# Kernel tuning notes

Hardware: AMD Instinct MI355X
Metric: run time of the kernel (lower is better)

The kernel has to match this reference:

```python
import jax, jax.numpy as jnp
import numpy as np

N_DROPOUT = 1      # init kwarg n_dropout
MIN_TOKENS = 10    # init kwarg min_tokens
# dynamic_dropout = False


def setup_inputs() -> dict:
    key = jax.random.key(0)
    k1, k2 = jax.random.split(key)
    B, S, V = 8192, 2048, 32000
    tokens = jax.random.randint(k1, (B, S), 1, V, dtype=jnp.int32)
    lengths = jax.random.randint(k2, (B,), 5, S + 1, dtype=jnp.int32)
    # contiguous prefix of positive token ids, 0-padded tail (as the module assumes)
    valid = jnp.arange(S, dtype=jnp.int32)[None, :] < lengths[:, None]
    input_ids = jnp.where(valid, tokens, 0)
    return {"input_ids": input_ids}


def reference(input_ids):
    # Vectorized equivalent of the per-row Python loop (training mode):
    # for every odd row with n_tokens >= MIN_TOKENS, zero N_DROPOUT random
    # token positions among the first n_tokens, then compact nonzeros left.
    B, S = input_ids.shape
    key = jax.random.key(42)

    n_tokens = jnp.sum(input_ids > 0, axis=1)  # [B]

    # random selection of N_DROPOUT distinct valid positions per row
    # (equivalent in distribution to randperm(n_tokens)[:N_DROPOUT])
    r = jax.random.uniform(key, (B, S))
    pos = jnp.arange(S)
    r = jnp.where(pos[None, :] < n_tokens[:, None], r, jnp.inf)
    _, drop_idx = jax.lax.top_k(-r, N_DROPOUT)  # [B, N_DROPOUT] smallest r
    drop_mask = jnp.zeros((B, S), dtype=bool).at[
        jnp.arange(B)[:, None], drop_idx
    ].set(True)

    apply_row = (jnp.arange(B) % 2 == 1) & (n_tokens >= MIN_TOKENS)  # [B]

    dropped = jnp.where(drop_mask & apply_row[:, None], 0, input_ids)

    # compaction: stable sort keys (zero-ness) -> nonzeros keep order, zeros go last
    order = jnp.argsort(dropped == 0, axis=1, stable=True)
    compacted = jnp.take_along_axis(dropped, order, axis=1)

    return jnp.where(apply_row[:, None], compacted, input_ids)
```

## Files before the change

### kernel.cpp

```cpp
#include <hip/hip_runtime.h>

#define PRNG_VARIANT 1

constexpr int S = 2048;
constexpr int BLOCK = 256;
constexpr int PER_THREAD = S / BLOCK;

__device__ __forceinline__ unsigned rotl32(unsigned x, int r) {
    return (x << r) | (x >> (32 - r));
}

__device__ __forceinline__ void threefry2x32_k42(unsigned c0, unsigned c1,
                                                 unsigned& o0, unsigned& o1) {
    const unsigned ks0 = 0u;
    const unsigned ks1 = 42u;
    const unsigned ks2 = 0x1BD11BDAu ^ ks0 ^ ks1;
    unsigned x0 = c0 + ks0;
    unsigned x1 = c1 + ks1;
#define TF_R4(a, b, c, d)                                   \
    x0 += x1; x1 = rotl32(x1, a); x1 ^= x0;                 \
    x0 += x1; x1 = rotl32(x1, b); x1 ^= x0;                 \
    x0 += x1; x1 = rotl32(x1, c); x1 ^= x0;                 \
    x0 += x1; x1 = rotl32(x1, d); x1 ^= x0;
    TF_R4(13, 15, 26, 6)   x0 += ks1; x1 += ks2 + 1u;
    TF_R4(17, 29, 16, 24)  x0 += ks2; x1 += ks0 + 2u;
    TF_R4(13, 15, 26, 6)   x0 += ks0; x1 += ks1 + 3u;
    TF_R4(17, 29, 16, 24)  x0 += ks1; x1 += ks2 + 4u;
    TF_R4(13, 15, 26, 6)   x0 += ks2; x1 += ks0 + 5u;
#undef TF_R4
    o0 = x0;
    o1 = x1;
}

__device__ __forceinline__ unsigned prng_bits(unsigned flat_idx, unsigned half) {
    unsigned o0, o1;
#if PRNG_VARIANT == 0
    threefry2x32_k42(0u, flat_idx, o0, o1);
    return o0;
#elif PRNG_VARIANT == 1
    threefry2x32_k42(0u, flat_idx, o0, o1);
    return o0 ^ o1;
#elif PRNG_VARIANT == 3
    threefry2x32_k42(0u, flat_idx, o0, o1);
    return o1;
#else
    if (flat_idx < half) {
        threefry2x32_k42(flat_idx, flat_idx + half, o0, o1);
        return o0;
    } else {
        threefry2x32_k42(flat_idx - half, flat_idx, o0, o1);
        return o1;
    }
#endif
}

__global__ __launch_bounds__(BLOCK) void random_dropout_kernel(
    const int* __restrict__ in, int* __restrict__ out, unsigned half_total) {
    __shared__ int row[S];
    __shared__ int wcnt[BLOCK / 64];
    __shared__ unsigned long long wmin[BLOCK / 64];
    __shared__ int s_ntok;
    __shared__ int s_drop;

    const int b = blockIdx.x;
    const size_t base = (size_t)b * S;
    const int4* vin = (const int4*)(in + base);
    int4* vout = (int4*)(out + base);
    const int tid = threadIdx.x;

    int4 v[2];
    int cnt = 0;
#pragma unroll
    for (int k = 0; k < 2; k++) {
        v[k] = vin[tid + k * BLOCK];
        ((int4*)row)[tid + k * BLOCK] = v[k];
        cnt += (v[k].x > 0) + (v[k].y > 0) + (v[k].z > 0) + (v[k].w > 0);
    }
#pragma unroll
    for (int off = 32; off; off >>= 1) cnt += __shfl_down(cnt, off, 64);
    if ((tid & 63) == 0) wcnt[tid >> 6] = cnt;
    __syncthreads();
    if (tid == 0) s_ntok = wcnt[0] + wcnt[1] + wcnt[2] + wcnt[3];
    __syncthreads();
    const int ntok = s_ntok;
    const bool apply = (b & 1) && (ntok >= 10);

    if (!apply) {
#pragma unroll
        for (int k = 0; k < 2; k++) vout[tid + k * BLOCK] = v[k];
        return;
    }

    unsigned long long best = ~0ull;
    for (int k = 0; k < PER_THREAD; k++) {
        const int s = tid + k * BLOCK;
        if (s >= ntok) break;
        const unsigned i = (unsigned)(b * S + s);
        const unsigned bits = prng_bits(i, half_total);
        const unsigned long long comb =
            ((unsigned long long)(bits >> 9) << 11) | (unsigned)s;
        best = comb < best ? comb : best;
    }
#pragma unroll
    for (int off = 32; off; off >>= 1) {
        const unsigned long long o = __shfl_down(best, off, 64);
        best = o < best ? o : best;
    }
    if ((tid & 63) == 0) wmin[tid >> 6] = best;
    __syncthreads();
    if (tid == 0) {
        unsigned long long m = wmin[0];
        m = wmin[1] < m ? wmin[1] : m;
        m = wmin[2] < m ? wmin[2] : m;
        m = wmin[3] < m ? wmin[3] : m;
        s_drop = (int)(m & 0x7FFull);
    }
    __syncthreads();
    const int drop = s_drop;

#pragma unroll
    for (int k = 0; k < 2; k++) {
        const int j4 = tid + k * BLOCK;
        const int jb = j4 * 4;
        int4 o;
        int* op = (int*)&o;
#pragma unroll
        for (int c = 0; c < 4; c++) {
            const int j = jb + c;
            int val;
            if (j < drop) val = row[j];
            else if (j < ntok - 1) val = row[j + 1];
            else val = 0;
            op[c] = val;
        }
        vout[j4] = o;
    }
}

extern "C" void kernel_launch(void* const* d_in, const int* in_sizes, int n_in,
                              void* d_out, int out_size, void* d_ws, size_t ws_size,
                              hipStream_t stream) {
    const int* in = (const int*)d_in[0];
    int* out = (int*)d_out;
    const int total = in_sizes[0];
    const int B = total / S;
    const unsigned half_total = (unsigned)(total / 2);
    random_dropout_kernel<<<B, BLOCK, 0, stream>>>(in, out, half_total);
}
```

Measured before the change: 122.2 us.

## Process one row per wavefront and replace shared-memory shifting with lane shuffles

Each 64-lane wave now owns a whole row, with four rows per block, so counting, the argmin reduction and broadcast use only wave shuffles and drop the shared memory and block barriers. The compaction shift is done in registers with cross-lane shuffles instead of a shared-memory row copy. The unused PRNG variants are removed. Each lane now holds 8 int4 values and runs up to 32 threefry evaluations serially, which raises register pressure and per-lane latency. The launch also assumes B is divisible by four.

Result: faster. 118.0 us (-3.4%).

```diff
diff --git a/kernel.cpp b/kernel.cpp
--- a/kernel.cpp
+++ b/kernel.cpp
@@ -1,22 +1,21 @@
 #include <hip/hip_runtime.h>
 
-#define PRNG_VARIANT 1
 
 constexpr int S = 2048;
 constexpr int BLOCK = 256;
-constexpr int PER_THREAD = S / BLOCK;
+constexpr int ROWS_PER_BLOCK = 4;
+constexpr int CHUNKS = S / 4 / 64;
 
 __device__ __forceinline__ unsigned rotl32(unsigned x, int r) {
     return (x << r) | (x >> (32 - r));
 }
 
-__device__ __forceinline__ void threefry2x32_k42(unsigned c0, unsigned c1,
-                                                 unsigned& o0, unsigned& o1) {
+__device__ __forceinline__ unsigned prng_bits(unsigned flat_idx) {
     const unsigned ks0 = 0u;
     const unsigned ks1 = 42u;
     const unsigned ks2 = 0x1BD11BDAu ^ ks0 ^ ks1;
-    unsigned x0 = c0 + ks0;
-    unsigned x1 = c1 + ks1;
+    unsigned x0 = 0u + ks0;
+    unsigned x1 = flat_idx + ks1;
 #define TF_R4(a, b, c, d)                                   \
     x0 += x1; x1 = rotl32(x1, a); x1 ^= x0;                 \
     x0 += x1; x1 = rotl32(x1, b); x1 ^= x0;                 \
@@ -28,75 +27,40 @@
     TF_R4(17, 29, 16, 24)  x0 += ks1; x1 += ks2 + 4u;
     TF_R4(13, 15, 26, 6)   x0 += ks2; x1 += ks0 + 5u;
 #undef TF_R4
-    o0 = x0;
-    o1 = x1;
-}
-
-__device__ __forceinline__ unsigned prng_bits(unsigned flat_idx, unsigned half) {
-    unsigned o0, o1;
-#if PRNG_VARIANT == 0
-    threefry2x32_k42(0u, flat_idx, o0, o1);
-    return o0;
-#elif PRNG_VARIANT == 1
-    threefry2x32_k42(0u, flat_idx, o0, o1);
-    return o0 ^ o1;
-#elif PRNG_VARIANT == 3
-    threefry2x32_k42(0u, flat_idx, o0, o1);
-    return o1;
-#else
-    if (flat_idx < half) {
-        threefry2x32_k42(flat_idx, flat_idx + half, o0, o1);
-        return o0;
-    } else {
-        threefry2x32_k42(flat_idx - half, flat_idx, o0, o1);
-        return o1;
-    }
-#endif
+    return x0 ^ x1;
 }
 
 __global__ __launch_bounds__(BLOCK) void random_dropout_kernel(
-    const int* __restrict__ in, int* __restrict__ out, unsigned half_total) {
-    __shared__ int row[S];
-    __shared__ int wcnt[BLOCK / 64];
-    __shared__ unsigned long long wmin[BLOCK / 64];
-    __shared__ int s_ntok;
-    __shared__ int s_drop;
-
-    const int b = blockIdx.x;
+    const int* __restrict__ in, int* __restrict__ out) {
+    const int wave = threadIdx.x >> 6;
+    const int lane = threadIdx.x & 63;
+    const int b = blockIdx.x * ROWS_PER_BLOCK + wave;
     const size_t base = (size_t)b * S;
     const int4* vin = (const int4*)(in + base);
     int4* vout = (int4*)(out + base);
-    const int tid = threadIdx.x;
 
-    int4 v[2];
+    int4 v[CHUNKS];
     int cnt = 0;
 #pragma unroll
-    for (int k = 0; k < 2; k++) {
-        v[k] = vin[tid + k * BLOCK];
-        ((int4*)row)[tid + k * BLOCK] = v[k];
+    for (int k = 0; k < CHUNKS; k++) {
+        v[k] = vin[lane + 64 * k];
         cnt += (v[k].x > 0) + (v[k].y > 0) + (v[k].z > 0) + (v[k].w > 0);
     }
 #pragma unroll
     for (int off = 32; off; off >>= 1) cnt += __shfl_down(cnt, off, 64);
-    if ((tid & 63) == 0) wcnt[tid >> 6] = cnt;
-    __syncthreads();
-    if (tid == 0) s_ntok = wcnt[0] + wcnt[1] + wcnt[2] + wcnt[3];
-    __syncthreads();
-    const int ntok = s_ntok;
+    const int ntok = __shfl(cnt, 0, 64);
+
     const bool apply = (b & 1) && (ntok >= 10);
-
     if (!apply) {
 #pragma unroll
-        for (int k = 0; k < 2; k++) vout[tid + k * BLOCK] = v[k];
+        for (int k = 0; k < CHUNKS; k++) vout[lane + 64 * k] = v[k];
         return;
     }
 
     unsigned long long best = ~0ull;
-    for (int k = 0; k < PER_THREAD; k++) {
-        const int s = tid + k * BLOCK;
-        if (s >= ntok) break;
-        const unsigned i = (unsigned)(b * S + s);
-        const unsigned bits = prng_bits(i, half_total);
+    const unsigned rowbase = (unsigned)b * (unsigned)S;
+    for (int s = lane; s < ntok; s += 64) {
+        const unsigned bits = prng_bits(rowbase + (unsigned)s);
         const unsigned long long comb =
             ((unsigned long long)(bits >> 9) << 11) | (unsigned)s;
         best = comb < best ? comb : best;
@@ -106,34 +70,26 @@
         const unsigned long long o = __shfl_down(best, off, 64);
         best = o < best ? o : best;
     }
-    if ((tid & 63) == 0) wmin[tid >> 6] = best;
-    __syncthreads();
-    if (tid == 0) {
-        unsigned long long m = wmin[0];
-        m = wmin[1] < m ? wmin[1] : m;
-        m = wmin[2] < m ? wmin[2] : m;
-        m = wmin[3] < m ? wmin[3] : m;
-        s_drop = (int)(m & 0x7FFull);
+    const unsigned long long m = __shfl(best, 0, 64);
+    const int drop = (int)(m & 0x7FFull);
+
+    int nx[CHUNKS];
+#pragma unroll
+    for (int k = 0; k < CHUNKS; k++) {
+        const int a = __shfl_down(v[k].x, 1, 64);
+        const int bb = (k < CHUNKS - 1) ? __shfl(v[k + 1].x, 0, 64) : 0;
+        nx[k] = (lane == 63) ? bb : a;
     }
-    __syncthreads();
-    const int drop = s_drop;
 
 #pragma unroll
-    for (int k = 0; k < 2; k++) {
-        const int j4 = tid + k * BLOCK;
-        const int jb = j4 * 4;
+    for (int k = 0; k < CHUNKS; k++) {
+        const int j0 = 4 * (lane + 64 * k);
         int4 o;
-        int* op = (int*)&o;
-#pragma unroll
-        for (int c = 0; c < 4; c++) {
-            const int j = jb + c;
-            int val;
-            if (j < drop) val = row[j];
-            else if (j < ntok - 1) val = row[j + 1];
-            else val = 0;
-            op[c] = val;
-        }
-        vout[j4] = o;
+        o.x = (j0 + 0 < drop) ? v[k].x : v[k].y;
+        o.y = (j0 + 1 < drop) ? v[k].y : v[k].z;
+        o.z = (j0 + 2 < drop) ? v[k].z : v[k].w;
+        o.w = (j0 + 3 < drop) ? v[k].w : nx[k];
+        vout[lane + 64 * k] = o;
     }
 }
 
@@ -144,6 +100,5 @@
     int* out = (int*)d_out;
     const int total = in_sizes[0];
     const int B = total / S;
-    const unsigned half_total = (unsigned)(total / 2);
-    random_dropout_kernel<<<B, BLOCK, 0, stream>>>(in, out, half_total);
+    random_dropout_kernel<<<B / ROWS_PER_BLOCK, BLOCK, 0, stream>>>(in, out);
 }
```
